# Optimization experiments

Measured on AMD Instinct MI355X. Metric: run time of the kernel, lower is better.

## Reference

```python
import jax, jax.numpy as jnp
import numpy as np

B, D = 4096, 128
TEMPERATURE = 0.2

def setup_inputs() -> dict:
    key = jax.random.key(0)
    k1, k2 = jax.random.split(key)
    z1 = jax.random.normal(k1, (B, D), dtype=jnp.float32)
    z2 = jax.random.normal(k2, (B, D), dtype=jnp.float32)
    return {"z1": z1, "z2": z2}

def reference(z1, z2):
    # single-process path: global batch == local batch
    gb = z1.shape[0]
    z = jnp.concatenate([z1, z2], axis=0)              # [2B, D]
    sim = jnp.matmul(z, z.T) / TEMPERATURE             # [2B, 2B]
    n = 2 * gb
    diag = jnp.eye(n, dtype=bool)
    sim = jnp.where(diag, jnp.finfo(sim.dtype).min, sim)
    targets = jnp.concatenate([jnp.arange(gb, n), jnp.arange(0, gb)])
    logp = jax.nn.log_softmax(sim, axis=-1)            # [2B, 2B]
    loss_all = -logp[jnp.arange(n), targets]           # [2B]
    # rank 0, world_size 1 -> idx_keep covers all rows
    return loss_all.mean()
```

## Files before the change

kernel.cpp:

```cpp
#include <hip/hip_runtime.h>
#include <stdint.h>

typedef unsigned short u16;
typedef unsigned int u32;

#define NTOT 8192
#define BH   4096
#define DD   128
#define COLSPLIT 8
#define COLS_PER_SPLIT (NTOT / COLSPLIT)
#define TILE_COLS 128
#define TILES_PER_SPLIT (COLS_PER_SPLIT / TILE_COLS)
#define ROWS_PER_BLOCK 128
#define ROWS_PER_WAVE 32
#define LDS_PITCH 136
#define NEG_INF (-3.0e38f)
#define SCALE_IN 2.68579144f
#define LN2F 0.6931471805599453f

typedef __bf16 bf16x8 __attribute__((ext_vector_type(8)));
typedef float  f32x4  __attribute__((ext_vector_type(4)));

__device__ __forceinline__ u16 f2bf(float f) {
  u32 u = __float_as_uint(f);
  return (u16)((u + 0x7fffu + ((u >> 16) & 1u)) >> 16);
}

__device__ __forceinline__ float fexp2(float x) {
#if __has_builtin(__builtin_amdgcn_exp2f)
  return __builtin_amdgcn_exp2f(x);
#else
  float r; asm("v_exp_f32 %0, %1" : "=v"(r) : "v"(x)); return r;
#endif
}

__global__ __launch_bounds__(256) void ntx_convert(
    const float* __restrict__ z1, const float* __restrict__ z2,
    u16* __restrict__ zb, float* __restrict__ out) {
  if (blockIdx.x == 0 && threadIdx.x == 0) out[0] = 0.f;
  const int i = (blockIdx.x * 256 + threadIdx.x) * 4;
  const int half = BH * DD;
  float4 v = (i < half) ? *reinterpret_cast<const float4*>(z1 + i)
                        : *reinterpret_cast<const float4*>(z2 + (i - half));
  u32 lo = (u32)f2bf(v.x * SCALE_IN) | ((u32)f2bf(v.y * SCALE_IN) << 16);
  u32 hi = (u32)f2bf(v.z * SCALE_IN) | ((u32)f2bf(v.w * SCALE_IN) << 16);
  uint2 o; o.x = lo; o.y = hi;
  *reinterpret_cast<uint2*>(zb + i) = o;
}

__global__ __launch_bounds__(256, 2) void ntx_main(
    const u16* __restrict__ zb,
    float* __restrict__ m_part, float* __restrict__ l_part,
    float* __restrict__ st_part) {
  __shared__ u16 lds_tile[TILE_COLS * LDS_PITCH];

  const int tid  = threadIdx.x;
  const int wave = tid >> 6;
  const int lane = tid & 63;
  const int l15  = lane & 15;
  const int q    = lane >> 4;

  const int rwave = blockIdx.x * ROWS_PER_BLOCK + wave * ROWS_PER_WAVE;
  const int split = blockIdx.y;
  const int col0  = split * COLS_PER_SPLIT;

  bf16x8 afrag[2][4];
#pragma unroll
  for (int rt = 0; rt < 2; ++rt)
#pragma unroll
    for (int kk = 0; kk < 4; ++kk) {
      const int r = rwave + rt * 16 + l15;
      afrag[rt][kk] = *reinterpret_cast<const bf16x8*>(zb + r * DD + kk * 32 + q * 8);
    }

  float m_run[2][4], l_run[2][4], stv[2][4];
#pragma unroll
  for (int rt = 0; rt < 2; ++rt)
#pragma unroll
    for (int r = 0; r < 4; ++r) { m_run[rt][r] = NEG_INF; l_run[rt][r] = 0.f; stv[rt][r] = NEG_INF; }

  for (int t = 0; t < TILES_PER_SPLIT; ++t) {
    const int ct0 = col0 + t * TILE_COLS;

    __syncthreads();
    {
      const uint4* src = reinterpret_cast<const uint4*>(zb + ct0 * DD);
#pragma unroll
      for (int i = 0; i < 8; ++i) {
        const int c   = tid + i * 256;
        const int col = c >> 4, w16 = c & 15;
        uint4 v = src[c];
        *reinterpret_cast<uint4*>(lds_tile + col * LDS_PITCH + w16 * 8) = v;
      }
    }
    __syncthreads();

    f32x4 acc[2][8];
#pragma unroll
    for (int rt = 0; rt < 2; ++rt)
#pragma unroll
      for (int cs = 0; cs < 8; ++cs) acc[rt][cs] = (f32x4){0.f, 0.f, 0.f, 0.f};

#pragma unroll
    for (int cs = 0; cs < 8; ++cs) {
      bf16x8 bfrag[4];
#pragma unroll
      for (int kk = 0; kk < 4; ++kk)
        bfrag[kk] = *reinterpret_cast<const bf16x8*>(
            lds_tile + (cs * 16 + l15) * LDS_PITCH + kk * 32 + q * 8);
#pragma unroll
      for (int rt = 0; rt < 2; ++rt)
#pragma unroll
        for (int kk = 0; kk < 4; ++kk)
          acc[rt][cs] = __builtin_amdgcn_mfma_f32_16x16x32_bf16(
              afrag[rt][kk], bfrag[kk], acc[rt][cs], 0, 0, 0);
    }

    const bool has_diag = (rwave >= ct0) && (rwave < ct0 + TILE_COLS);
    const int  trow     = rwave ^ BH;
    const bool has_tgt  = (trow >= ct0) && (trow < ct0 + TILE_COLS);
    if (has_diag || has_tgt) {
#pragma unroll
      for (int rt = 0; rt < 2; ++rt)
#pragma unroll
        for (int r = 0; r < 4; ++r) {
          const int grow = rwave + rt * 16 + q * 4 + r;
#pragma unroll
          for (int cs = 0; cs < 8; ++cs) {
            const int gcol = ct0 + cs * 16 + l15;
            float v = acc[rt][cs][r];
            if (gcol == (grow ^ BH)) stv[rt][r] = fmaxf(stv[rt][r], v);
            if (gcol == grow) acc[rt][cs][r] = NEG_INF;
          }
        }
    }

#pragma unroll
    for (int rt = 0; rt < 2; ++rt)
#pragma unroll
      for (int r = 0; r < 4; ++r) {
        float mx = acc[rt][0][r];
#pragma unroll
        for (int cs = 1; cs < 8; ++cs) mx = fmaxf(mx, acc[rt][cs][r]);
        const float mnew = fmaxf(m_run[rt][r], mx);
        float s = 0.f;
#pragma unroll
        for (int cs = 0; cs < 8; ++cs) s += fexp2(acc[rt][cs][r] - mnew);
        l_run[rt][r] = l_run[rt][r] * fexp2(m_run[rt][r] - mnew) + s;
        m_run[rt][r] = mnew;
      }
  }

#pragma unroll
  for (int rt = 0; rt < 2; ++rt)
#pragma unroll
    for (int r = 0; r < 4; ++r) {
      float m = m_run[rt][r], l = l_run[rt][r];
#pragma unroll
      for (int off = 1; off < 16; off <<= 1) {
        const float mo = __shfl_xor(m, off, 64);
        const float lo = __shfl_xor(l, off, 64);
        const float mn = fmaxf(m, mo);
        l = l * fexp2(m - mn) + lo * fexp2(mo - mn);
        m = mn;
      }
      float sv = stv[rt][r];
#pragma unroll
      for (int off = 1; off < 16; off <<= 1) sv = fmaxf(sv, __shfl_xor(sv, off, 64));
      if (l15 == 0) {
        const int grow = rwave + rt * 16 + q * 4 + r;
        m_part[split * NTOT + grow] = m;
        l_part[split * NTOT + grow] = l;
        const int tcol = grow ^ BH;
        if (tcol >= col0 && tcol < col0 + COLS_PER_SPLIT) st_part[grow] = sv;
      }
    }
}

__global__ __launch_bounds__(256) void ntx_finish(
    const float* __restrict__ m_part, const float* __restrict__ l_part,
    const float* __restrict__ st_part, float* __restrict__ out) {
  const int row = blockIdx.x * 256 + threadIdx.x;
  float m = NEG_INF;
#pragma unroll
  for (int s = 0; s < COLSPLIT; ++s) m = fmaxf(m, m_part[s * NTOT + row]);
  float l = 0.f;
#pragma unroll
  for (int s = 0; s < COLSPLIT; ++s) l += l_part[s * NTOT + row] * fexp2(m_part[s * NTOT + row] - m);
  float loss = LN2F * (m + __log2f(l) - st_part[row]);

#pragma unroll
  for (int off = 32; off >= 1; off >>= 1) loss += __shfl_xor(loss, off, 64);
  __shared__ float wsum[4];
  if ((threadIdx.x & 63) == 0) wsum[threadIdx.x >> 6] = loss;
  __syncthreads();
  if (threadIdx.x == 0) {
    float s = wsum[0] + wsum[1] + wsum[2] + wsum[3];
    atomicAdd(out, s * (1.0f / NTOT));
  }
}

extern "C" void kernel_launch(void* const* d_in, const int* in_sizes, int n_in,
                              void* d_out, int out_size, void* d_ws, size_t ws_size,
                              hipStream_t stream) {
  const float* z1 = (const float*)d_in[0];
  const float* z2 = (const float*)d_in[1];
  float* out = (float*)d_out;

  char* ws = (char*)d_ws;
  u16*   zb      = (u16*)ws;
  float* m_part  = (float*)(ws + (size_t)NTOT * DD * 2);
  float* l_part  = m_part + COLSPLIT * NTOT;
  float* st_part = l_part + COLSPLIT * NTOT;

  ntx_convert<<<dim3((NTOT * DD) / (256 * 4)), dim3(256), 0, stream>>>(z1, z2, zb, out);
  ntx_main<<<dim3(NTOT / ROWS_PER_BLOCK, COLSPLIT), dim3(256), 0, stream>>>(
      zb, m_part, l_part, st_part);
  ntx_finish<<<dim3(NTOT / 256), dim3(256), 0, stream>>>(m_part, l_part, st_part, out);
}
```

Before: 86.06 us.

## Split block tile into 2x2 wave grid over rows and columns

Each wave now computes a 64-row by 64-column sub-tile instead of 32 rows by 128 columns, with waves arranged 2x2 across the block's rows and the shared column tile. This halves the LDS B-fragment reads per MFMA, since each B fragment is reused across four row tiles instead of two. Each column half writes its own softmax partials, so the partial buffers and the finish kernel double to 16 splits. The cost is more A-fragment registers per wave, extra workspace, and more partials to merge in the finish kernel.

```diff
diff --git a/kernel.cpp b/kernel.cpp
--- a/kernel.cpp
+++ b/kernel.cpp
@@ -12,7 +12,6 @@
 #define TILE_COLS 128
 #define TILES_PER_SPLIT (COLS_PER_SPLIT / TILE_COLS)
 #define ROWS_PER_BLOCK 128
-#define ROWS_PER_WAVE 32
 #define LDS_PITCH 136
 #define NEG_INF (-3.0e38f)
 #define SCALE_IN 2.68579144f
@@ -60,22 +59,26 @@
   const int l15  = lane & 15;
   const int q    = lane >> 4;
 
-  const int rwave = blockIdx.x * ROWS_PER_BLOCK + wave * ROWS_PER_WAVE;
+  const int rowhalf = wave & 1;
+  const int colhalf = wave >> 1;
+  const int cwl     = colhalf * 64;
+
+  const int rwave = blockIdx.x * ROWS_PER_BLOCK + rowhalf * 64;
   const int split = blockIdx.y;
   const int col0  = split * COLS_PER_SPLIT;
 
-  bf16x8 afrag[2][4];
-#pragma unroll
-  for (int rt = 0; rt < 2; ++rt)
+  bf16x8 afrag[4][4];
+#pragma unroll
+  for (int rt = 0; rt < 4; ++rt)
 #pragma unroll
     for (int kk = 0; kk < 4; ++kk) {
       const int r = rwave + rt * 16 + l15;
       afrag[rt][kk] = *reinterpret_cast<const bf16x8*>(zb + r * DD + kk * 32 + q * 8);
     }
 
-  float m_run[2][4], l_run[2][4], stv[2][4];
-#pragma unroll
-  for (int rt = 0; rt < 2; ++rt)
+  float m_run[4][4], l_run[4][4], stv[4][4];
+#pragma unroll
+  for (int rt = 0; rt < 4; ++rt)
 #pragma unroll
     for (int r = 0; r < 4; ++r) { m_run[rt][r] = NEG_INF; l_run[rt][r] = 0.f; stv[rt][r] = NEG_INF; }
 
@@ -95,39 +98,39 @@
     }
     __syncthreads();
 
-    f32x4 acc[2][8];
-#pragma unroll
-    for (int rt = 0; rt < 2; ++rt)
-#pragma unroll
-      for (int cs = 0; cs < 8; ++cs) acc[rt][cs] = (f32x4){0.f, 0.f, 0.f, 0.f};
-
-#pragma unroll
-    for (int cs = 0; cs < 8; ++cs) {
+    f32x4 acc[4][4];
+#pragma unroll
+    for (int rt = 0; rt < 4; ++rt)
+#pragma unroll
+      for (int cs = 0; cs < 4; ++cs) acc[rt][cs] = (f32x4){0.f, 0.f, 0.f, 0.f};
+
+#pragma unroll
+    for (int cs = 0; cs < 4; ++cs) {
       bf16x8 bfrag[4];
 #pragma unroll
       for (int kk = 0; kk < 4; ++kk)
         bfrag[kk] = *reinterpret_cast<const bf16x8*>(
-            lds_tile + (cs * 16 + l15) * LDS_PITCH + kk * 32 + q * 8);
-#pragma unroll
-      for (int rt = 0; rt < 2; ++rt)
+            lds_tile + (cwl + cs * 16 + l15) * LDS_PITCH + kk * 32 + q * 8);
+#pragma unroll
+      for (int rt = 0; rt < 4; ++rt)
 #pragma unroll
         for (int kk = 0; kk < 4; ++kk)
           acc[rt][cs] = __builtin_amdgcn_mfma_f32_16x16x32_bf16(
               afrag[rt][kk], bfrag[kk], acc[rt][cs], 0, 0, 0);
     }
 
-    const bool has_diag = (rwave >= ct0) && (rwave < ct0 + TILE_COLS);
-    const int  trow     = rwave ^ BH;
-    const bool has_tgt  = (trow >= ct0) && (trow < ct0 + TILE_COLS);
+    const int  ccol0    = ct0 + cwl;
+    const bool has_diag = (ccol0 == rwave);
+    const bool has_tgt  = (ccol0 == (rwave ^ BH));
     if (has_diag || has_tgt) {
 #pragma unroll
-      for (int rt = 0; rt < 2; ++rt)
+      for (int rt = 0; rt < 4; ++rt)
 #pragma unroll
         for (int r = 0; r < 4; ++r) {
           const int grow = rwave + rt * 16 + q * 4 + r;
 #pragma unroll
-          for (int cs = 0; cs < 8; ++cs) {
-            const int gcol = ct0 + cs * 16 + l15;
+          for (int cs = 0; cs < 4; ++cs) {
+            const int gcol = ccol0 + cs * 16 + l15;
             float v = acc[rt][cs][r];
             if (gcol == (grow ^ BH)) stv[rt][r] = fmaxf(stv[rt][r], v);
             if (gcol == grow) acc[rt][cs][r] = NEG_INF;
@@ -136,23 +139,23 @@
     }
 
 #pragma unroll
-    for (int rt = 0; rt < 2; ++rt)
+    for (int rt = 0; rt < 4; ++rt)
 #pragma unroll
       for (int r = 0; r < 4; ++r) {
         float mx = acc[rt][0][r];
 #pragma unroll
-        for (int cs = 1; cs < 8; ++cs) mx = fmaxf(mx, acc[rt][cs][r]);
+        for (int cs = 1; cs < 4; ++cs) mx = fmaxf(mx, acc[rt][cs][r]);
         const float mnew = fmaxf(m_run[rt][r], mx);
         float s = 0.f;
 #pragma unroll
-        for (int cs = 0; cs < 8; ++cs) s += fexp2(acc[rt][cs][r] - mnew);
+        for (int cs = 0; cs < 4; ++cs) s += fexp2(acc[rt][cs][r] - mnew);
         l_run[rt][r] = l_run[rt][r] * fexp2(m_run[rt][r] - mnew) + s;
         m_run[rt][r] = mnew;
       }
   }
 
 #pragma unroll
-  for (int rt = 0; rt < 2; ++rt)
+  for (int rt = 0; rt < 4; ++rt)
 #pragma unroll
     for (int r = 0; r < 4; ++r) {
       float m = m_run[rt][r], l = l_run[rt][r];
@@ -169,10 +172,13 @@
       for (int off = 1; off < 16; off <<= 1) sv = fmaxf(sv, __shfl_xor(sv, off, 64));
       if (l15 == 0) {
         const int grow = rwave + rt * 16 + q * 4 + r;
-        m_part[split * NTOT + grow] = m;
-        l_part[split * NTOT + grow] = l;
+        const int sp   = split * 2 + colhalf;
+        m_part[sp * NTOT + grow] = m;
+        l_part[sp * NTOT + grow] = l;
         const int tcol = grow ^ BH;
-        if (tcol >= col0 && tcol < col0 + COLS_PER_SPLIT) st_part[grow] = sv;
+        if (tcol >= col0 && tcol < col0 + COLS_PER_SPLIT &&
+            (((tcol >> 6) & 1) == colhalf))
+          st_part[grow] = sv;
       }
     }
 }
@@ -183,10 +189,11 @@
   const int row = blockIdx.x * 256 + threadIdx.x;
   float m = NEG_INF;
 #pragma unroll
-  for (int s = 0; s < COLSPLIT; ++s) m = fmaxf(m, m_part[s * NTOT + row]);
+  for (int s = 0; s < COLSPLIT * 2; ++s) m = fmaxf(m, m_part[s * NTOT + row]);
   float l = 0.f;
 #pragma unroll
-  for (int s = 0; s < COLSPLIT; ++s) l += l_part[s * NTOT + row] * fexp2(m_part[s * NTOT + row] - m);
+  for (int s = 0; s < COLSPLIT * 2; ++s)
+    l += l_part[s * NTOT + row] * fexp2(m_part[s * NTOT + row] - m);
   float loss = LN2F * (m + __log2f(l) - st_part[row]);
 
 #pragma unroll
@@ -210,8 +217,8 @@
   char* ws = (char*)d_ws;
   u16*   zb      = (u16*)ws;
   float* m_part  = (float*)(ws + (size_t)NTOT * DD * 2);
-  float* l_part  = m_part + COLSPLIT * NTOT;
-  float* st_part = l_part + COLSPLIT * NTOT;
+  float* l_part  = m_part + COLSPLIT * 2 * NTOT;
+  float* st_part = l_part + COLSPLIT * 2 * NTOT;
 
   ntx_convert<<<dim3((NTOT * DD) / (256 * 4)), dim3(256), 0, stream>>>(z1, z2, zb, out);
   ntx_main<<<dim3(NTOT / ROWS_PER_BLOCK, COLSPLIT), dim3(256), 0, stream>>>(
```

Result: slower. 90.85 us (+5.6%).
